# Performance work log

Measured on AMD Instinct MI355X. Metric: run time of the kernel, lower is better.

The kernel has to match this reference:

```python
import jax, jax.numpy as jnp
import numpy as np

N = 50000      # nodes
E = 800000     # edges (avg degree 16)
IN_DIM = 256
OUT_DIM = 64
HEADS = 4
P_L = 0.1      # freq='low' slope


def setup_inputs() -> dict:
    key = jax.random.key(0)
    ks = jax.random.split(key, 12)
    h = jax.random.normal(ks[0], (N, IN_DIM), dtype=jnp.float32)
    src = jax.random.randint(ks[1], (E,), 0, N, dtype=jnp.int32)
    dst = jax.random.randint(ks[2], (E,), 0, N, dtype=jnp.int32)
    d = jax.random.uniform(ks[3], (N,), dtype=jnp.float32)  # degree norm per node
    s_in = 1.0 / np.sqrt(IN_DIM)
    s_d = 1.0 / np.sqrt(OUT_DIM)
    W_in = jax.random.normal(ks[4], (IN_DIM, HEADS * OUT_DIM), dtype=jnp.float32) * s_in
    b_in = jnp.zeros((HEADS * OUT_DIM,), dtype=jnp.float32)
    W_att = jax.random.normal(ks[5], (HEADS, OUT_DIM, OUT_DIM), dtype=jnp.float32) * s_d
    b_att = jnp.zeros((HEADS, OUT_DIM), dtype=jnp.float32)
    W_g = jax.random.normal(ks[6], (HEADS, 2 * OUT_DIM), dtype=jnp.float32) * s_d
    b_g = jnp.zeros((HEADS,), dtype=jnp.float32)
    W_out = jax.random.normal(ks[7], (HEADS * OUT_DIM, OUT_DIM), dtype=jnp.float32) * s_d
    b_out = jnp.zeros((OUT_DIM,), dtype=jnp.float32)
    return {"h": h, "src": src, "dst": dst, "d": d,
            "W_in": W_in, "b_in": b_in, "W_att": W_att, "b_att": b_att,
            "W_g": W_g, "b_g": b_g, "W_out": W_out, "b_out": b_out}


def reference(h, src, dst, d, W_in, b_in, W_att, b_att, W_g, b_g, W_out, b_out):
    # node transform: [N, H, D]  (dropout is identity in eval mode)
    hh = jax.nn.relu(h @ W_in + b_in).reshape(-1, HEADS, OUT_DIM)
    # per-head att_gate applied at node level (same math as per-edge, cheaper)
    a = jnp.einsum('nhd,hde->nhe', hh, W_att) + b_att           # [N, H, D]
    # gate linear on concat([dst_a, src_a]) split into the two halves of W_g
    g_dst = jnp.einsum('nhd,hd->nh', a, W_g[:, :OUT_DIM])        # [N, H]
    g_src = jnp.einsum('nhd,hd->nh', a, W_g[:, OUT_DIM:])        # [N, H]
    _h = g_dst[dst] + g_src[src] + b_g                           # [E, H]
    # freq='low': relu(where(_h>0, _h, -p_l*_h)) == where(_h>0, _h, -p_l*_h)
    g = jnp.where(_h > 0, _h, -P_L * _h)
    alpha = g * (d[dst] * d[src])[:, None]                       # [E, H]
    msg = hh[src] * alpha[..., None]                             # [E, H, D]
    z = jax.ops.segment_sum(msg, dst, num_segments=N)            # [N, H, D]
    return z.reshape(-1, HEADS * OUT_DIM) @ W_out + b_out        # [N, D]
```

## Files before the change

kernel.cpp:

```cpp
#include <hip/hip_runtime.h>
#include <hip/hip_bf16.h>

#define N_NODES 50000
#define N_EDGES 800000
#define IN_DIM 256
#define OUT_DIM 64
#define HEADS 4
#define HD 256
#define P_L 0.1f
#define TILE_N 64
#define CAP 64
#define OVCAP 4096

typedef __attribute__((ext_vector_type(8))) short bf16x8;
typedef __attribute__((ext_vector_type(4))) float f32x4;

static __device__ __forceinline__ short f2bf(float f) {
    __hip_bfloat16 b = __float2bfloat16(f);
    return *(short*)&b;
}

__global__ __launch_bounds__(256) void prep_kernel(
    const float* __restrict__ W_att, const float* __restrict__ b_att,
    const float* __restrict__ W_g,
    const float* __restrict__ W_in, const float* __restrict__ W_out,
    short* __restrict__ W_bt, short* __restrict__ W_obt2,
    float* __restrict__ v_dst, float* __restrict__ v_src,
    float* __restrict__ c_dst, float* __restrict__ c_src) {
    int b = blockIdx.x, t = threadIdx.x;
    if (b < 256) {
        W_bt[t * 256 + b] = f2bf(W_in[b * 256 + t]);
    } else if (b < 320) {
        int flat = (b - 256) * 256 + t;
        int k = flat & 63, oc = (flat >> 6) & 63, h = flat >> 12;
        W_obt2[flat] = f2bf(W_out[(h * 64 + k) * 64 + oc]);
    } else {
        int h = t >> 6, dd = t & 63;
        float sd = 0.f, ss = 0.f;
        for (int e = 0; e < 64; ++e) {
            float w = W_att[h * 4096 + dd * 64 + e];
            sd += w * W_g[h * 128 + e];
            ss += w * W_g[h * 128 + 64 + e];
        }
        v_dst[t] = sd;
        v_src[t] = ss;
        if (dd == 0) {
            float cd = 0.f, cs = 0.f;
            for (int e = 0; e < 64; ++e) {
                float bb = b_att[h * 64 + e];
                cd += bb * W_g[h * 128 + e];
                cs += bb * W_g[h * 128 + 64 + e];
            }
            c_dst[h] = cd;
            c_src[h] = cs;
        }
    }
}

__global__ __launch_bounds__(256) void fill_kernel(
    const int* __restrict__ src, const int* __restrict__ dst,
    int* __restrict__ cursor, int* __restrict__ bucket_src,
    int* __restrict__ ov_list, int* __restrict__ ov_count) {
    int e = blockIdx.x * 256 + threadIdx.x;
    if (e >= N_EDGES) return;
    int n = dst[e];
    int pos = atomicAdd(&cursor[n], 1);
    if (pos < CAP) {
        bucket_src[(size_t)n * CAP + pos] = src[e];
    } else {
        int oi = atomicAdd(ov_count, 1);
        if (oi < OVCAP) ov_list[oi] = e;
    }
}

__global__ __launch_bounds__(256) void node_mfma_kernel(
    const float* __restrict__ hin, const short* __restrict__ W_bt,
    const short* __restrict__ W_obt2, const float* __restrict__ b_in,
    const float* __restrict__ v_dst, const float* __restrict__ v_src,
    const float* __restrict__ c_dst, const float* __restrict__ c_src,
    const float* __restrict__ dnorm,
    __hip_bfloat16* __restrict__ y, float* __restrict__ gd,
    float2* __restrict__ gsp) {
    __shared__ short A_lds[TILE_N * 256];
    int t = threadIdx.x;
    int n0 = blockIdx.x * TILE_N;
    bool full = (n0 + TILE_N) <= N_NODES;

    #pragma unroll
    for (int rr = 0; rr < 4; ++rr) {
        int r = rr * 16 + (t >> 4), c0 = (t & 15) * 16;
        int row = n0 + r;
        if (row > N_NODES - 1) row = N_NODES - 1;
        const float* hp = hin + (size_t)row * IN_DIM + c0;
        float fv[16];
        *(float4*)&fv[0]  = *(const float4*)(hp + 0);
        *(float4*)&fv[4]  = *(const float4*)(hp + 4);
        *(float4*)&fv[8]  = *(const float4*)(hp + 8);
        *(float4*)&fv[12] = *(const float4*)(hp + 12);
        short sv[16];
        #pragma unroll
        for (int j = 0; j < 16; ++j) sv[j] = f2bf(fv[j]);
        int swz = (r & 7) << 3;
        int base = r * 256 + c0;
        *(bf16x8*)&A_lds[(base + 0) ^ swz] = *(bf16x8*)&sv[0];
        *(bf16x8*)&A_lds[(base + 8) ^ swz] = *(bf16x8*)&sv[8];
    }
    __syncthreads();

    int l = t & 63, w = t >> 6;
    int lr = l & 15, lg = l >> 4;
    int aswz = (lr & 7) << 3;

    f32x4 acc[4][4];
    #pragma unroll
    for (int rt = 0; rt < 4; ++rt)
        #pragma unroll
        for (int ct = 0; ct < 4; ++ct) acc[rt][ct] = (f32x4){0.f, 0.f, 0.f, 0.f};

    #pragma unroll
    for (int ks = 0; ks < 8; ++ks) {
        bf16x8 bfrag[4], afrag[4];
        #pragma unroll
        for (int ct = 0; ct < 4; ++ct)
            bfrag[ct] = *(const bf16x8*)(W_bt + (size_t)(w * 64 + ct * 16 + lr) * 256 + ks * 32 + lg * 8);
        #pragma unroll
        for (int rt = 0; rt < 4; ++rt)
            afrag[rt] = *(bf16x8*)&A_lds[((rt * 16 + lr) * 256 + ks * 32 + lg * 8) ^ aswz];
        #pragma unroll
        for (int rt = 0; rt < 4; ++rt)
            #pragma unroll
            for (int ct = 0; ct < 4; ++ct)
                acc[rt][ct] = __builtin_amdgcn_mfma_f32_16x16x32_bf16(afrag[rt], bfrag[ct], acc[rt][ct], 0, 0, 0);
    }

    int col[4];
    float vd[4], vs[4], bi[4];
    #pragma unroll
    for (int ct = 0; ct < 4; ++ct) {
        col[ct] = w * 64 + ct * 16 + lr;
        bi[ct] = b_in[col[ct]];
        vd[ct] = v_dst[col[ct]];
        vs[ct] = v_src[col[ct]];
    }
    float pd[4][4], ps[4][4];
    #pragma unroll
    for (int rt = 0; rt < 4; ++rt)
        #pragma unroll
        for (int r = 0; r < 4; ++r) { pd[rt][r] = 0.f; ps[rt][r] = 0.f; }
    #pragma unroll
    for (int rt = 0; rt < 4; ++rt)
        #pragma unroll
        for (int ct = 0; ct < 4; ++ct)
            #pragma unroll
            for (int r = 0; r < 4; ++r) {
                float v = fmaxf(acc[rt][ct][r] + bi[ct], 0.f);
                acc[rt][ct][r] = v;
                pd[rt][r] += v * vd[ct];
                ps[rt][r] += v * vs[ct];
            }
    #pragma unroll
    for (int rt = 0; rt < 4; ++rt)
        #pragma unroll
        for (int r = 0; r < 4; ++r) {
            #pragma unroll
            for (int off = 1; off < 16; off <<= 1) {
                pd[rt][r] += __shfl_xor(pd[rt][r], off, 64);
                ps[rt][r] += __shfl_xor(ps[rt][r], off, 64);
            }
        }
    if (lr == 0) {
        float cd = c_dst[w], cs = c_src[w];
        #pragma unroll
        for (int rt = 0; rt < 4; ++rt)
            #pragma unroll
            for (int r = 0; r < 4; ++r) {
                int m = rt * 16 + lg * 4 + r;
                if (full || (n0 + m) < N_NODES) {
                    gd[(n0 + m) * HEADS + w] = pd[rt][r] + cd;
                    gsp[(n0 + m) * HEADS + w] =
                        make_float2(ps[rt][r] + cs, dnorm[n0 + m]);
                }
            }
    }

    __syncthreads();
    #pragma unroll
    for (int rt = 0; rt < 4; ++rt)
        #pragma unroll
        for (int ct = 0; ct < 4; ++ct)
            #pragma unroll
            for (int r = 0; r < 4; ++r) {
                int m = rt * 16 + lg * 4 + r;
                int idx = m * 256 + col[ct];
                A_lds[idx ^ (((lg * 4 + r) & 7) << 3)] = f2bf(acc[rt][ct][r]);
            }
    #pragma unroll
    for (int rt = 0; rt < 4; ++rt)
        #pragma unroll
        for (int ct = 0; ct < 4; ++ct) acc[rt][ct] = (f32x4){0.f, 0.f, 0.f, 0.f};
    __syncthreads();

    #pragma unroll
    for (int ks = 0; ks < 2; ++ks) {
        bf16x8 bfrag[4], afrag[4];
        #pragma unroll
        for (int ct = 0; ct < 4; ++ct)
            bfrag[ct] = *(const bf16x8*)(W_obt2 + (size_t)(w * 64 + ct * 16 + lr) * 64 + ks * 32 + lg * 8);
        #pragma unroll
        for (int rt = 0; rt < 4; ++rt)
            afrag[rt] = *(bf16x8*)&A_lds[((rt * 16 + lr) * 256 + w * 64 + ks * 32 + lg * 8) ^ aswz];
        #pragma unroll
        for (int rt = 0; rt < 4; ++rt)
            #pragma unroll
            for (int ct = 0; ct < 4; ++ct)
                acc[rt][ct] = __builtin_amdgcn_mfma_f32_16x16x32_bf16(afrag[rt], bfrag[ct], acc[rt][ct], 0, 0, 0);
    }
    #pragma unroll
    for (int rt = 0; rt < 4; ++rt)
        #pragma unroll
        for (int ct = 0; ct < 4; ++ct)
            #pragma unroll
            for (int r = 0; r < 4; ++r) {
                int m = rt * 16 + lg * 4 + r;
                if (full || (n0 + m) < N_NODES)
                    y[(size_t)(n0 + m) * HD + w * 64 + ct * 16 + lr] =
                        __float2bfloat16(acc[rt][ct][r]);
            }
}

__global__ __launch_bounds__(256) void agg_kernel(
    const int* __restrict__ bucket_src, const int* __restrict__ cursor,
    const int* __restrict__ src, const int* __restrict__ dst,
    const int* __restrict__ ov_list, const int* __restrict__ ov_count,
    const float* __restrict__ dnorm, const float* __restrict__ b_g,
    const __hip_bfloat16* __restrict__ y, const float* __restrict__ gd,
    const float2* __restrict__ gsp, const float* __restrict__ b_out,
    float* __restrict__ out) {
    int t = threadIdx.x;
    int wv = t >> 6, lane = t & 63;
    int half = lane >> 5, sl = lane & 31;
    int n = blockIdx.x * 8 + wv * 2 + half;
    int head = sl >> 3;
    int deg = cursor[n];
    if (deg > CAP) deg = CAP;
    float dn = dnorm[n];
    float gdh = gd[n * HEADS + head] + b_g[head];
    int degmax = max(deg, __shfl_xor(deg, 32, 64));

    const uint4* yb = (const uint4*)y;
    const int* bp = bucket_src + (size_t)n * CAP;
    float a[8];
    #pragma unroll
    for (int j = 0; j < 8; ++j) a[j] = 0.f;

    for (int i = 0; i < degmax; i += 8) {
        int sarr[8];
        #pragma unroll
        for (int j = 0; j < 8; ++j) {
            int e = i + j;
            sarr[j] = (e < deg) ? bp[e] : -1;
        }
        float2 gg[8];
        uint4 v[8];
        #pragma unroll
        for (int j = 0; j < 8; ++j) {
            int s = sarr[j] < 0 ? 0 : sarr[j];
            gg[j] = gsp[s * HEADS + head];
            v[j] = yb[(size_t)s * 32 + sl];
        }
        #pragma unroll
        for (int j = 0; j < 8; ++j) {
            float _h = gdh + gg[j].x;
            float g = _h > 0.f ? _h : -P_L * _h;
            float al = (sarr[j] < 0) ? 0.f : g * dn * gg[j].y;
            a[0] += __uint_as_float(v[j].x << 16) * al;
            a[1] += __uint_as_float(v[j].x & 0xffff0000u) * al;
            a[2] += __uint_as_float(v[j].y << 16) * al;
            a[3] += __uint_as_float(v[j].y & 0xffff0000u) * al;
            a[4] += __uint_as_float(v[j].z << 16) * al;
            a[5] += __uint_as_float(v[j].z & 0xffff0000u) * al;
            a[6] += __uint_as_float(v[j].w << 16) * al;
            a[7] += __uint_as_float(v[j].w & 0xffff0000u) * al;
        }
    }

    int cnt = *ov_count;
    if (cnt > 0) {
        if (cnt > OVCAP) cnt = OVCAP;
        for (int j = 0; j < cnt; ++j) {
            int e = ov_list[j];
            if (dst[e] == n) {
                int s = src[e];
                float2 gg = gsp[s * HEADS + head];
                float _h = gdh + gg.x;
                float g = _h > 0.f ? _h : -P_L * _h;
                float al = g * dn * gg.y;
                uint4 vv = yb[(size_t)s * 32 + sl];
                a[0] += __uint_as_float(vv.x << 16) * al;
                a[1] += __uint_as_float(vv.x & 0xffff0000u) * al;
                a[2] += __uint_as_float(vv.y << 16) * al;
                a[3] += __uint_as_float(vv.y & 0xffff0000u) * al;
                a[4] += __uint_as_float(vv.z << 16) * al;
                a[5] += __uint_as_float(vv.z & 0xffff0000u) * al;
                a[6] += __uint_as_float(vv.w << 16) * al;
                a[7] += __uint_as_float(vv.w & 0xffff0000u) * al;
            }
        }
    }

    #pragma unroll
    for (int j = 0; j < 8; ++j) {
        a[j] += __shfl_xor(a[j], 8, 64);
        a[j] += __shfl_xor(a[j], 16, 64);
    }
    if (sl < 8) {
        float4 b0 = *(const float4*)&b_out[sl * 8];
        float4 b1 = *(const float4*)&b_out[sl * 8 + 4];
        float4 o0, o1;
        o0.x = a[0] + b0.x; o0.y = a[1] + b0.y; o0.z = a[2] + b0.z; o0.w = a[3] + b0.w;
        o1.x = a[4] + b1.x; o1.y = a[5] + b1.y; o1.z = a[6] + b1.z; o1.w = a[7] + b1.w;
        *(float4*)&out[(size_t)n * OUT_DIM + sl * 8] = o0;
        *(float4*)&out[(size_t)n * OUT_DIM + sl * 8 + 4] = o1;
    }
}

extern "C" void kernel_launch(void* const* d_in, const int* in_sizes, int n_in,
                              void* d_out, int out_size, void* d_ws, size_t ws_size,
                              hipStream_t stream) {
    const float* h     = (const float*)d_in[0];
    const int*   src   = (const int*)d_in[1];
    const int*   dst   = (const int*)d_in[2];
    const float* dnorm = (const float*)d_in[3];
    const float* W_in  = (const float*)d_in[4];
    const float* b_in  = (const float*)d_in[5];
    const float* W_att = (const float*)d_in[6];
    const float* b_att = (const float*)d_in[7];
    const float* W_g   = (const float*)d_in[8];
    const float* b_g   = (const float*)d_in[9];
    const float* W_out = (const float*)d_in[10];
    const float* b_out = (const float*)d_in[11];
    float* out = (float*)d_out;

    char* ws = (char*)d_ws;
    __hip_bfloat16* y = (__hip_bfloat16*)ws;
    ws += (size_t)N_NODES * HD * sizeof(__hip_bfloat16);
    float* gd     = (float*)ws;  ws += (size_t)N_NODES * HEADS * sizeof(float);
    float2* gsp   = (float2*)ws; ws += (size_t)N_NODES * HEADS * sizeof(float2);
    float* v_dst  = (float*)ws;  ws += 256 * sizeof(float);
    float* v_src  = (float*)ws;  ws += 256 * sizeof(float);
    float* c_dst  = (float*)ws;  ws += 16;
    float* c_src  = (float*)ws;  ws += 16;
    int* cursor     = (int*)ws;  ws += (size_t)N_NODES * sizeof(int);
    int* ov_count   = (int*)ws;  ws += 16;
    int* ov_list    = (int*)ws;  ws += OVCAP * sizeof(int);
    int* bucket_src = (int*)ws;  ws += (size_t)N_NODES * CAP * sizeof(int);
    short* W_bt     = (short*)ws; ws += 256 * 256 * sizeof(short);
    short* W_obt2   = (short*)ws;

    hipMemsetAsync(cursor, 0, (size_t)N_NODES * sizeof(int), stream);
    hipMemsetAsync(ov_count, 0, sizeof(int), stream);

    prep_kernel<<<321, 256, 0, stream>>>(W_att, b_att, W_g, W_in, W_out,
                                         W_bt, W_obt2, v_dst, v_src, c_dst, c_src);
    fill_kernel<<<(N_EDGES + 255) / 256, 256, 0, stream>>>(src, dst, cursor, bucket_src,
                                                           ov_list, ov_count);
    node_mfma_kernel<<<(N_NODES + TILE_N - 1) / TILE_N, 256, 0, stream>>>(
        h, W_bt, W_obt2, b_in, v_dst, v_src, c_dst, c_src, dnorm, y, gd, gsp);
    agg_kernel<<<N_NODES / 8, 256, 0, stream>>>(bucket_src, cursor, src, dst,
                                                ov_list, ov_count, dnorm, b_g,
                                                y, gd, gsp, b_out, out);
}
```

Measured before the change: 175.1 us.

## Split node MFMA kernel in two, batch fill atomics, prefetch bucket indices

Splits the fused node kernel into hh_kernel, which computes the relu'd hidden projection and gate scalars and writes the swizzled bf16 tile to a global scratch buffer, and y_kernel, which reloads that buffer and applies the W_out projection. This likely aims to cut per-kernel register and LDS pressure, at the cost of an extra launch and a round trip of about 25 MB through global memory. fill_kernel now handles four edges per thread so more loads are in flight before the atomics. agg_kernel prefetches the next eight bucket source indices while processing the current batch to hide index-load latency.

```diff
diff --git a/kernel.cpp b/kernel.cpp
--- a/kernel.cpp
+++ b/kernel.cpp
@@ -2,6 +2,7 @@
 #include <hip/hip_bf16.h>
 
 #define N_NODES 50000
+#define N_PAD 50048
 #define N_EDGES 800000
 #define IN_DIM 256
 #define OUT_DIM 64
@@ -61,25 +62,37 @@
     const int* __restrict__ src, const int* __restrict__ dst,
     int* __restrict__ cursor, int* __restrict__ bucket_src,
     int* __restrict__ ov_list, int* __restrict__ ov_count) {
-    int e = blockIdx.x * 256 + threadIdx.x;
-    if (e >= N_EDGES) return;
-    int n = dst[e];
-    int pos = atomicAdd(&cursor[n], 1);
-    if (pos < CAP) {
-        bucket_src[(size_t)n * CAP + pos] = src[e];
-    } else {
-        int oi = atomicAdd(ov_count, 1);
-        if (oi < OVCAP) ov_list[oi] = e;
-    }
-}
-
-__global__ __launch_bounds__(256) void node_mfma_kernel(
+    int base = blockIdx.x * 1024 + threadIdx.x;
+    int d4[4], s4[4];
+    #pragma unroll
+    for (int j = 0; j < 4; ++j) {
+        int e = base + j * 256;
+        bool ok = e < N_EDGES;
+        d4[j] = ok ? dst[e] : -1;
+        s4[j] = ok ? src[e] : 0;
+    }
+    #pragma unroll
+    for (int j = 0; j < 4; ++j) {
+        if (d4[j] >= 0) {
+            int pos = atomicAdd(&cursor[d4[j]], 1);
+            if (pos < CAP) {
+                bucket_src[(size_t)d4[j] * CAP + pos] = s4[j];
+            } else {
+                int e = base + j * 256;
+                int oi = atomicAdd(ov_count, 1);
+                if (oi < OVCAP) ov_list[oi] = e;
+            }
+        }
+    }
+}
+
+__global__ __launch_bounds__(256) void hh_kernel(
     const float* __restrict__ hin, const short* __restrict__ W_bt,
-    const short* __restrict__ W_obt2, const float* __restrict__ b_in,
+    const float* __restrict__ b_in,
     const float* __restrict__ v_dst, const float* __restrict__ v_src,
     const float* __restrict__ c_dst, const float* __restrict__ c_src,
     const float* __restrict__ dnorm,
-    __hip_bfloat16* __restrict__ y, float* __restrict__ gd,
+    short* __restrict__ hh_swz, float* __restrict__ gd,
     float2* __restrict__ gsp) {
     __shared__ short A_lds[TILE_N * 256];
     int t = threadIdx.x;
@@ -194,11 +207,30 @@
                 int idx = m * 256 + col[ct];
                 A_lds[idx ^ (((lg * 4 + r) & 7) << 3)] = f2bf(acc[rt][ct][r]);
             }
+    __syncthreads();
+    short* hg = hh_swz + (size_t)n0 * 256;
+    #pragma unroll
+    for (int i = 0; i < 8; ++i) {
+        int sidx = t * 8 + i * 2048;
+        *(bf16x8*)&hg[sidx] = *(bf16x8*)&A_lds[sidx];
+    }
+}
+
+__global__ __launch_bounds__(256) void y_kernel(
+    const short* __restrict__ hh_swz, const short* __restrict__ W_obt2,
+    __hip_bfloat16* __restrict__ y) {
+    int t = threadIdx.x;
+    int n0 = blockIdx.x * TILE_N;
+    bool full = (n0 + TILE_N) <= N_NODES;
+    int l = t & 63, w = t >> 6;
+    int lr = l & 15, lg = l >> 4;
+    int aswz = (lr & 7) << 3;
+
+    f32x4 acc[4][4];
     #pragma unroll
     for (int rt = 0; rt < 4; ++rt)
         #pragma unroll
         for (int ct = 0; ct < 4; ++ct) acc[rt][ct] = (f32x4){0.f, 0.f, 0.f, 0.f};
-    __syncthreads();
 
     #pragma unroll
     for (int ks = 0; ks < 2; ++ks) {
@@ -207,8 +239,11 @@
         for (int ct = 0; ct < 4; ++ct)
             bfrag[ct] = *(const bf16x8*)(W_obt2 + (size_t)(w * 64 + ct * 16 + lr) * 64 + ks * 32 + lg * 8);
         #pragma unroll
-        for (int rt = 0; rt < 4; ++rt)
-            afrag[rt] = *(bf16x8*)&A_lds[((rt * 16 + lr) * 256 + w * 64 + ks * 32 + lg * 8) ^ aswz];
+        for (int rt = 0; rt < 4; ++rt) {
+            size_t row = (size_t)(n0 + rt * 16 + lr);
+            int off = (w * 64 + ks * 32 + lg * 8) ^ aswz;
+            afrag[rt] = *(const bf16x8*)(hh_swz + row * 256 + off);
+        }
         #pragma unroll
         for (int rt = 0; rt < 4; ++rt)
             #pragma unroll
@@ -253,18 +288,26 @@
     #pragma unroll
     for (int j = 0; j < 8; ++j) a[j] = 0.f;
 
+    int snxt[8];
+    #pragma unroll
+    for (int j = 0; j < 8; ++j) snxt[j] = (j < deg) ? bp[j] : -1;
+
     for (int i = 0; i < degmax; i += 8) {
-        int sarr[8];
-        #pragma unroll
-        for (int j = 0; j < 8; ++j) {
-            int e = i + j;
-            sarr[j] = (e < deg) ? bp[e] : -1;
+        int scur[8];
+        #pragma unroll
+        for (int j = 0; j < 8; ++j) scur[j] = snxt[j];
+        if (i + 8 < degmax) {
+            #pragma unroll
+            for (int j = 0; j < 8; ++j) {
+                int e = i + 8 + j;
+                snxt[j] = (e < deg) ? bp[e] : -1;
+            }
         }
         float2 gg[8];
         uint4 v[8];
         #pragma unroll
         for (int j = 0; j < 8; ++j) {
-            int s = sarr[j] < 0 ? 0 : sarr[j];
+            int s = scur[j] < 0 ? 0 : scur[j];
             gg[j] = gsp[s * HEADS + head];
             v[j] = yb[(size_t)s * 32 + sl];
         }
@@ -272,7 +315,7 @@
         for (int j = 0; j < 8; ++j) {
             float _h = gdh + gg[j].x;
             float g = _h > 0.f ? _h : -P_L * _h;
-            float al = (sarr[j] < 0) ? 0.f : g * dn * gg[j].y;
+            float al = (scur[j] < 0) ? 0.f : g * dn * gg[j].y;
             a[0] += __uint_as_float(v[j].x << 16) * al;
             a[1] += __uint_as_float(v[j].x & 0xffff0000u) * al;
             a[2] += __uint_as_float(v[j].y << 16) * al;
@@ -344,6 +387,8 @@
     char* ws = (char*)d_ws;
     __hip_bfloat16* y = (__hip_bfloat16*)ws;
     ws += (size_t)N_NODES * HD * sizeof(__hip_bfloat16);
+    short* hh_swz = (short*)ws;
+    ws += (size_t)N_PAD * HD * sizeof(short);
     float* gd     = (float*)ws;  ws += (size_t)N_NODES * HEADS * sizeof(float);
     float2* gsp   = (float2*)ws; ws += (size_t)N_NODES * HEADS * sizeof(float2);
     float* v_dst  = (float*)ws;  ws += 256 * sizeof(float);
@@ -362,10 +407,11 @@
 
     prep_kernel<<<321, 256, 0, stream>>>(W_att, b_att, W_g, W_in, W_out,
                                          W_bt, W_obt2, v_dst, v_src, c_dst, c_src);
-    fill_kernel<<<(N_EDGES + 255) / 256, 256, 0, stream>>>(src, dst, cursor, bucket_src,
-                                                           ov_list, ov_count);
-    node_mfma_kernel<<<(N_NODES + TILE_N - 1) / TILE_N, 256, 0, stream>>>(
-        h, W_bt, W_obt2, b_in, v_dst, v_src, c_dst, c_src, dnorm, y, gd, gsp);
+    fill_kernel<<<(N_EDGES + 1023) / 1024, 256, 0, stream>>>(src, dst, cursor, bucket_src,
+                                                             ov_list, ov_count);
+    hh_kernel<<<(N_NODES + TILE_N - 1) / TILE_N, 256, 0, stream>>>(
+        h, W_bt, b_in, v_dst, v_src, c_dst, c_src, dnorm, hh_swz, gd, gsp);
+    y_kernel<<<(N_NODES + TILE_N - 1) / TILE_N, 256, 0, stream>>>(hh_swz, W_obt2, y);
     agg_kernel<<<N_NODES / 8, 256, 0, stream>>>(bucket_src, cursor, src, dst,
                                                 ov_list, ov_count, dnorm, b_g,
                                                 y, gd, gsp, b_out, out);
```

Measured after the change: 186.4 us. 1.06x slower.
